# Optimization experiments

Measured on AMD Instinct MI355X. Metric: run time of the kernel, lower is better.

The kernel has to match this reference:

```python
import jax, jax.numpy as jnp
import numpy as np


def setup_inputs() -> dict:
    key = jax.random.key(0)
    k1, k2, k3, k4 = jax.random.split(key, 4)
    N, Ck, Cv, T, H, W = 8, 128, 512, 8, 30, 30
    return {
        "q_key": jax.random.normal(k1, (N, Ck, H, W), dtype=jnp.float32),
        "q_val": jax.random.normal(k2, (N, Cv, H, W), dtype=jnp.float32),
        "m_key": jax.random.normal(k3, (N, Ck, T, H, W), dtype=jnp.float32),
        "m_val": jax.random.normal(k4, (N, Cv, T, H, W), dtype=jnp.float32),
    }


def reference(q_key, q_val, m_key, m_val):
    N, Ck, H, W = q_key.shape
    _, Cv, T, Hm, Wm = m_val.shape
    qk = q_key.reshape(N, Ck, H * W)            # n c q
    mk = m_key.reshape(N, Ck, T * Hm * Wm)      # n c m
    # affinity [n, q, m], scaled by 1/sqrt(Ck)
    aff = jnp.einsum("ncq,ncm->nqm", qk, mk) * (Ck ** -0.5)
    # NOTE: softmax over the QUERY axis (axis=1), per the original module
    attn = jax.nn.softmax(aff, axis=1)
    mv = m_val.reshape(N, Cv, T * Hm * Wm)      # n c m
    mapped = jnp.einsum("nqm,ncm->ncq", attn, mv).reshape(N, Cv, Hm, Wm)
    return jnp.concatenate([q_val, mapped], axis=1)  # [N, 2*Cv, H, W]
```

## Files before the change

kernel.cpp:

```cpp
#include <hip/hip_runtime.h>
#include <stdint.h>

#define N_  8
#define CK  128
#define CV  512
#define HW  900
#define M_  7200
#define QK_SCALE 0.08838834764831845f

typedef __attribute__((ext_vector_type(8))) short  short8;
typedef __attribute__((ext_vector_type(4))) float  floatx4;
typedef __attribute__((ext_vector_type(4))) unsigned int   uintx4;
typedef __attribute__((ext_vector_type(4))) unsigned short ushortx4;

__device__ __forceinline__ uint16_t f32_to_bf16(float x) {
    union { float f; uint32_t u; } v; v.f = x;
    return (uint16_t)((v.u + 0x7FFFu + ((v.u >> 16) & 1u)) >> 16);
}

__device__ __forceinline__ void gload_lds16(const uint16_t* g, short* l) {
    __builtin_amdgcn_global_load_lds(
        (const __attribute__((address_space(1))) void*)g,
        (__attribute__((address_space(3))) void*)l,
        16, 0, 0);
}

#define WAITV(n) asm volatile("s_waitcnt vmcnt(" #n ")" ::: "memory")
#define BARRIER() do { __builtin_amdgcn_sched_barrier(0); \
                       __builtin_amdgcn_s_barrier(); \
                       __builtin_amdgcn_sched_barrier(0); } while (0)

__global__ void k_zero(float* __restrict__ p) {
    int i = blockIdx.x * 256 + threadIdx.x;
    if (i < N_ * M_) p[i] = 0.f;
}

__global__ __launch_bounds__(256) void k_copy_qval(const float* __restrict__ qv,
                                                   float* __restrict__ out) {
    unsigned i = blockIdx.x * 256 + threadIdx.x;
    unsigned e = i * 4u;
    unsigned n = e / (CV * HW);
    unsigned off = e - n * (CV * HW);
    *(floatx4*)&out[(size_t)n * (2 * CV * HW) + off] = *(const floatx4*)&qv[e];
}

__global__ __launch_bounds__(256) void k_trans(const float* __restrict__ in,
                                               uint16_t* __restrict__ outp, int L) {
    __shared__ float tile[32][33];
    const int tx = threadIdx.x & 31;
    const int ty = threadIdx.x >> 5;
    const int l0 = blockIdx.x * 32;
    const int c0 = blockIdx.y * 32;
    const int n  = blockIdx.z;
    const float* src = in + (size_t)n * CK * L;
    uint16_t* dst = outp + (size_t)n * L * CK;
#pragma unroll
    for (int p = 0; p < 4; p++) {
        int c = c0 + p * 8 + ty;
        int l = l0 + tx;
        float v = 0.f;
        if (l < L) v = src[(size_t)c * L + l];
        tile[p * 8 + ty][tx] = v;
    }
    __syncthreads();
#pragma unroll
    for (int p = 0; p < 4; p++) {
        int l = l0 + p * 8 + ty;
        int c = c0 + tx;
        if (l < L) dst[(size_t)l * CK + c] = f32_to_bf16(tile[tx][p * 8 + ty]);
    }
}

#define K1_TS 144

__global__ __launch_bounds__(256) void k1_gemm_exp(
    const uint16_t* __restrict__ qkT,
    const uint16_t* __restrict__ mkT,
    uint16_t* __restrict__ E,
    float* __restrict__ dsum)
{
    __shared__ __align__(16) short smem[32768];
    __shared__ float colsum[128];

    const int bid = blockIdx.x + 57 * (blockIdx.y + 8 * blockIdx.z);
    const int swz = (bid & 7) * 456 + (bid >> 3);
    const int mb   = swz % 57;
    const int rest = swz / 57;
    const int m0 = mb * 128;
    const int q0 = (rest & 7) * 128;
    const int n  = rest >> 3;
    const int tid = threadIdx.x;

    if (tid < 128) colsum[tid] = 0.f;

    const int lane = tid & 63;
    const int wid  = tid >> 6;
    const int wq   = (wid >> 1) << 6;
    const int wm   = (wid & 1) << 6;
    const int fr   = lane & 15;
    const int quad = lane >> 4;

    const int ca = wid * 2;
    const int rr = lane >> 2;
    const int cc = (lane & 3) * 8;

    const uint16_t* Ab = qkT + (size_t)n * HW * CK;
    const uint16_t* Bb = mkT + (size_t)n * M_ * CK;
    const uint16_t* A0p = Ab + (size_t)(q0 + ca * 16 + rr) * CK + cc;
    const uint16_t* A1p = A0p + 16 * CK;
    const uint16_t* B0p = Bb + (size_t)(m0 + ca * 16 + rr) * CK + cc;
    const uint16_t* B1p = B0p + 16 * CK;

    floatx4 acc[4][4];
#pragma unroll
    for (int a = 0; a < 4; a++)
#pragma unroll
        for (int b = 0; b < 4; b++) acc[a][b] = (floatx4){0.f, 0.f, 0.f, 0.f};

#define K1_STAGE(buf, ko) do { \
    short* dA = smem + (buf) * 8192 + ca * 512; \
    short* dB = dA + 4096; \
    gload_lds16(A0p + (ko), dA); \
    gload_lds16(A1p + (ko), dA + 512); \
    gload_lds16(B0p + (ko), dB); \
    gload_lds16(B1p + (ko), dB + 512); \
} while (0)

#define K1_COMPUTE(buf) do { \
    const short* bA = smem + (buf) * 8192; \
    const short* bB = bA + 4096; \
    const int k0 = quad * 8; \
    short8 af[4], bfr[4]; \
    _Pragma("unroll") \
    for (int t = 0; t < 4; t++) \
        af[t] = *(const short8*)&bA[(wq + t * 16 + fr) * 32 + k0]; \
    _Pragma("unroll") \
    for (int t = 0; t < 4; t++) \
        bfr[t] = *(const short8*)&bB[(wm + t * 16 + fr) * 32 + k0]; \
    _Pragma("unroll") \
    for (int tq = 0; tq < 4; tq++) \
        _Pragma("unroll") \
        for (int tm = 0; tm < 4; tm++) \
            acc[tq][tm] = __builtin_amdgcn_mfma_f32_16x16x32_bf16( \
                af[tq], bfr[tm], acc[tq][tm], 0, 0, 0); \
} while (0)

    K1_STAGE(0, 0); K1_STAGE(1, 32); K1_STAGE(2, 64);
    WAITV(8); BARRIER(); K1_STAGE(3, 96); K1_COMPUTE(0);
    WAITV(8); BARRIER(); K1_COMPUTE(1);
    WAITV(4); BARRIER(); K1_COMPUTE(2);
    WAITV(0); BARRIER(); K1_COMPUTE(3);

    __syncthreads();
    float cs[4] = {0.f, 0.f, 0.f, 0.f};
#pragma unroll
    for (int tq = 0; tq < 4; tq++) {
#pragma unroll
        for (int tm = 0; tm < 4; tm++) {
            const int col = wm + tm * 16 + fr;
#pragma unroll
            for (int i = 0; i < 4; i++) {
                const int row = wq + tq * 16 + quad * 4 + i;
                float e = __expf(acc[tq][tm][i] * QK_SCALE);
                if (q0 + row < HW) cs[tm] += e;
                smem[row * K1_TS + col] = (short)f32_to_bf16(e);
            }
        }
    }
#pragma unroll
    for (int tm = 0; tm < 4; tm++) {
        float s = cs[tm];
        s += __shfl_xor(s, 16, 64);
        s += __shfl_xor(s, 32, 64);
        if (quad == 0) atomicAdd(&colsum[wm + tm * 16 + fr], s);
    }
    __syncthreads();

    uint16_t* En = E + (size_t)n * HW * M_;
#pragma unroll
    for (int j = 0; j < 8; j++) {
        int idx = tid + j * 256;
        int r   = idx >> 4;
        int c8  = (idx & 15) * 8;
        if (q0 + r < HW && m0 + c8 + 8 <= M_) {
            uintx4 v = *(const uintx4*)&smem[r * K1_TS + c8];
            *(uintx4*)&En[(size_t)(q0 + r) * M_ + m0 + c8] = v;
        }
    }
    if (tid < 128) {
        const int gm = m0 + tid;
        if (gm < M_) atomicAdd(&dsum[(size_t)n * M_ + gm], colsum[tid]);
    }
#undef K1_STAGE
#undef K1_COMPUTE
}

__global__ __launch_bounds__(256) void k_mvs(
    const float* __restrict__ mval,
    const float* __restrict__ dsum,
    uint16_t* __restrict__ mvs)
{
    unsigned i = blockIdx.x * 256 + threadIdx.x;
    unsigned base = i * 4u;
    unsigned n = base / (unsigned)(CV * M_);
    unsigned m = base % (unsigned)M_;
    floatx4 v = *(const floatx4*)&mval[base];
    floatx4 d = *(const floatx4*)&dsum[n * (unsigned)M_ + m];
    ushortx4 o;
    o[0] = f32_to_bf16(v[0] * (1.0f / d[0]));
    o[1] = f32_to_bf16(v[1] * (1.0f / d[1]));
    o[2] = f32_to_bf16(v[2] * (1.0f / d[2]));
    o[3] = f32_to_bf16(v[3] * (1.0f / d[3]));
    *(ushortx4*)&mvs[base] = o;
}

#define K2_NT 225

__global__ __launch_bounds__(256) void k2_hyb(
    const uint16_t* __restrict__ mvs,
    const uint16_t* __restrict__ E,
    float* __restrict__ out)
{
    __shared__ __align__(16) short ldsA[3 * 4096];

    const int bid = blockIdx.x + 8 * (blockIdx.y + 4 * blockIdx.z);
    const int swz = (bid & 7) * 32 + (bid >> 3);
    const int c0 = (swz & 3) << 7;
    const int q0 = ((swz >> 2) & 7) << 7;
    const int n  = swz >> 5;

    const int tid  = threadIdx.x;
    const int lane = tid & 63;
    const int wid  = tid >> 6;
    const int wc   = (wid >> 1) << 6;
    const int wq   = (wid & 1) << 6;
    const int fr   = lane & 15;
    const int quad = lane >> 4;

    const int ca = wid * 2;
    const int rr = lane >> 2;
    const int cc = (lane & 3) * 8;
    const uint16_t* A0p = mvs + (size_t)(n * CV + c0 + ca * 16 + rr) * M_ + cc;
    const uint16_t* A1p = A0p + (size_t)16 * M_;

    const uint16_t* En = E + (size_t)n * HW * M_;
    const uint16_t* Bp0 = En + (size_t)(q0 + wq +  0 + fr) * M_ + quad * 8;
    const uint16_t* Bp1 = En + (size_t)(q0 + wq + 16 + fr) * M_ + quad * 8;
    const uint16_t* Bp2 = En + (size_t)(q0 + wq + 32 + fr) * M_ + quad * 8;
    const uint16_t* Bp3 = En + (size_t)(q0 + wq + 48 + fr) * M_ + quad * 8;

    floatx4 acc[4][4];
#pragma unroll
    for (int a = 0; a < 4; a++)
#pragma unroll
        for (int b = 0; b < 4; b++) acc[a][b] = (floatx4){0.f, 0.f, 0.f, 0.f};

    short8 breg0[4], breg1[4], breg2[4];

#define K2_STAGE_A(buf, mo) do { \
    gload_lds16(A0p + (mo), ldsA + (buf) * 4096 + ca * 512); \
    gload_lds16(A1p + (mo), ldsA + (buf) * 4096 + ca * 512 + 512); \
} while (0)

#define K2_LOAD_B(brg, mo) do { \
    brg[0] = *(const short8*)(Bp0 + (mo)); \
    brg[1] = *(const short8*)(Bp1 + (mo)); \
    brg[2] = *(const short8*)(Bp2 + (mo)); \
    brg[3] = *(const short8*)(Bp3 + (mo)); \
} while (0)

#define K2_COMPUTE(bA, brg) do { \
    const short* pA = ldsA + (bA) * 4096; \
    short8 af[4]; \
    _Pragma("unroll") \
    for (int t = 0; t < 4; t++) \
        af[t] = *(const short8*)&pA[(wc + t * 16 + fr) * 32 + quad * 8]; \
    _Pragma("unroll") \
    for (int tc = 0; tc < 4; tc++) \
        _Pragma("unroll") \
        for (int tq = 0; tq < 4; tq++) \
            acc[tc][tq] = __builtin_amdgcn_mfma_f32_16x16x32_bf16( \
                af[tc], brg[tq], acc[tc][tq], 0, 0, 0); \
} while (0)

    K2_STAGE_A(0, 0);  K2_LOAD_B(breg0, 0);
    K2_STAGE_A(1, 32); K2_LOAD_B(breg1, 32);

    int mo = 64;
    for (int s = 0; s < 74; s++) {
        WAITV(10); BARRIER();
        K2_STAGE_A(2, mo); K2_LOAD_B(breg2, mo); K2_COMPUTE(0, breg0);
        mo += 32;
        WAITV(10); BARRIER();
        K2_STAGE_A(0, mo); K2_LOAD_B(breg0, mo); K2_COMPUTE(1, breg1);
        mo += 32;
        WAITV(10); BARRIER();
        K2_STAGE_A(1, mo); K2_LOAD_B(breg1, mo); K2_COMPUTE(2, breg2);
        mo += 32;
    }
    WAITV(10); BARRIER();
    K2_STAGE_A(2, mo); K2_LOAD_B(breg2, mo); K2_COMPUTE(0, breg0);
    WAITV(10); BARRIER();
    K2_COMPUTE(1, breg1);
    WAITV(4); BARRIER();
    K2_COMPUTE(2, breg2);

    float* On = out + (size_t)n * (2 * CV * HW) + (size_t)CV * HW;
#pragma unroll
    for (int tc = 0; tc < 4; tc++) {
#pragma unroll
        for (int tq = 0; tq < 4; tq++) {
            const int gq = q0 + wq + tq * 16 + fr;
            if (gq < HW) {
#pragma unroll
                for (int i = 0; i < 4; i++) {
                    const int gc = c0 + wc + tc * 16 + quad * 4 + i;
                    On[(size_t)gc * HW + gq] = acc[tc][tq][i];
                }
            }
        }
    }
#undef K2_STAGE_A
#undef K2_LOAD_B
#undef K2_COMPUTE
}

extern "C" void kernel_launch(void* const* d_in, const int* in_sizes, int n_in,
                              void* d_out, int out_size, void* d_ws, size_t ws_size,
                              hipStream_t stream) {
    const float* qkey = (const float*)d_in[0];
    const float* qval = (const float*)d_in[1];
    const float* mkey = (const float*)d_in[2];
    const float* mval = (const float*)d_in[3];
    float* out = (float*)d_out;

    char* ws = (char*)d_ws;
    uint16_t* E        = (uint16_t*)ws;
    float*    dsum     = (float*)(ws + 103680000);
    uint16_t* mvs      = (uint16_t*)(ws + 104140800);
    uint16_t* qkT      = (uint16_t*)(ws + 163123200);
    uint16_t* mkT      = (uint16_t*)(ws + 163123200 + 1843200);

    (void)in_sizes; (void)n_in; (void)out_size; (void)ws_size;

    k_zero<<<dim3((N_ * M_ + 255) / 256), 256, 0, stream>>>(dsum);
    k_copy_qval<<<dim3((N_ * CV * HW) / 4 / 256), 256, 0, stream>>>(qval, out);
    k_trans<<<dim3(29, 4, N_), 256, 0, stream>>>(qkey, qkT, HW);
    k_trans<<<dim3(225, 4, N_), 256, 0, stream>>>(mkey, mkT, M_);
    k1_gemm_exp<<<dim3(57, 8, N_), 256, 0, stream>>>(qkT, mkT, E, dsum);
    k_mvs<<<dim3((N_ * CV * M_) / 4 / 256), 256, 0, stream>>>(mval, dsum, mvs);
    k2_hyb<<<dim3(8, 4, 8), 256, 0, stream>>>(mvs, E, out);
}
```

Baseline: 471.9 us.

## Split second GEMM along M into three partials and fuse prep kernels

The second GEMM (attention times values) launched only 256 blocks, so it is now split along the memory dimension into three chunks of 2400. Each chunk writes fp32 partials to workspace, and a new reduce kernel sums them into the output. That gives 768 blocks for better occupancy across the many CUs, at the cost of extra partial write/read traffic and one more launch. Separately, the zero, copy and two transpose kernels are merged into one launch to cut launch overhead. The partials buffer reuses the qkT/mkT workspace region, which is safe because those are consumed before k2 runs.

Result: faster. 431.5 us (-8.6%).

```diff
diff --git a/kernel.cpp b/kernel.cpp
--- a/kernel.cpp
+++ b/kernel.cpp
@@ -30,30 +30,16 @@
                        __builtin_amdgcn_s_barrier(); \
                        __builtin_amdgcn_sched_barrier(0); } while (0)
 
-__global__ void k_zero(float* __restrict__ p) {
-    int i = blockIdx.x * 256 + threadIdx.x;
-    if (i < N_ * M_) p[i] = 0.f;
-}
-
-__global__ __launch_bounds__(256) void k_copy_qval(const float* __restrict__ qv,
-                                                   float* __restrict__ out) {
-    unsigned i = blockIdx.x * 256 + threadIdx.x;
-    unsigned e = i * 4u;
-    unsigned n = e / (CV * HW);
-    unsigned off = e - n * (CV * HW);
-    *(floatx4*)&out[(size_t)n * (2 * CV * HW) + off] = *(const floatx4*)&qv[e];
-}
-
-__global__ __launch_bounds__(256) void k_trans(const float* __restrict__ in,
-                                               uint16_t* __restrict__ outp, int L) {
+__device__ __forceinline__ void trans_body(const float* __restrict__ in,
+                                           uint16_t* __restrict__ outp, int L,
+                                           int bx, int by, int bz, int tid) {
     __shared__ float tile[32][33];
-    const int tx = threadIdx.x & 31;
-    const int ty = threadIdx.x >> 5;
-    const int l0 = blockIdx.x * 32;
-    const int c0 = blockIdx.y * 32;
-    const int n  = blockIdx.z;
-    const float* src = in + (size_t)n * CK * L;
-    uint16_t* dst = outp + (size_t)n * L * CK;
+    const int tx = tid & 31;
+    const int ty = tid >> 5;
+    const int l0 = bx * 32;
+    const int c0 = by * 32;
+    const float* src = in + (size_t)bz * CK * L;
+    uint16_t* dst = outp + (size_t)bz * L * CK;
 #pragma unroll
     for (int p = 0; p < 4; p++) {
         int c = c0 + p * 8 + ty;
@@ -68,6 +54,33 @@
         int l = l0 + p * 8 + ty;
         int c = c0 + tx;
         if (l < L) dst[(size_t)l * CK + c] = f32_to_bf16(tile[tx][p * 8 + ty]);
+    }
+}
+
+__global__ __launch_bounds__(256) void k_prep(
+    const float* __restrict__ qkey, const float* __restrict__ mkey,
+    const float* __restrict__ qval, float* __restrict__ out,
+    uint16_t* __restrict__ qkT, uint16_t* __restrict__ mkT,
+    float* __restrict__ dsum)
+{
+    const int b = blockIdx.x;
+    const int tid = threadIdx.x;
+    if (b < 928) {
+        trans_body(qkey, qkT, HW, b % 29, (b / 29) & 3, b / 116, tid);
+    } else if (b < 8128) {
+        const int bb = b - 928;
+        trans_body(mkey, mkT, M_, bb % 225, (bb / 225) & 3, bb / 900, tid);
+    } else if (b < 11728) {
+        const int bb = b - 8128;
+        unsigned i = (unsigned)bb * 256 + tid;
+        unsigned e = i * 4u;
+        unsigned n = e / (CV * HW);
+        unsigned off = e - n * (CV * HW);
+        *(floatx4*)&out[(size_t)n * (2 * CV * HW) + off] = *(const floatx4*)&qval[e];
+    } else {
+        const int bb = b - 11728;
+        int i = bb * 256 + tid;
+        if (i < N_ * M_) dsum[i] = 0.f;
     }
 }
 
@@ -214,20 +227,24 @@
     *(ushortx4*)&mvs[base] = o;
 }
 
-#define K2_NT 225
-
-__global__ __launch_bounds__(256) void k2_hyb(
+#define K2_SPLITS 3
+#define K2_BK 32
+#define K2_STEPS 75
+
+__global__ __launch_bounds__(256, 3) void k2_split3b(
     const uint16_t* __restrict__ mvs,
     const uint16_t* __restrict__ E,
-    float* __restrict__ out)
+    float* __restrict__ partials)
 {
     __shared__ __align__(16) short ldsA[3 * 4096];
 
     const int bid = blockIdx.x + 8 * (blockIdx.y + 4 * blockIdx.z);
-    const int swz = (bid & 7) * 32 + (bid >> 3);
+    const int swz = (bid & 7) * 96 + (bid >> 3);
     const int c0 = (swz & 3) << 7;
     const int q0 = ((swz >> 2) & 7) << 7;
-    const int n  = swz >> 5;
+    const int nz = swz >> 5;
+    const int n     = nz / K2_SPLITS;
+    const int split = nz - n * K2_SPLITS;
 
     const int tid  = threadIdx.x;
     const int lane = tid & 63;
@@ -240,10 +257,11 @@
     const int ca = wid * 2;
     const int rr = lane >> 2;
     const int cc = (lane & 3) * 8;
-    const uint16_t* A0p = mvs + (size_t)(n * CV + c0 + ca * 16 + rr) * M_ + cc;
+    const uint16_t* A0p = mvs + (size_t)(n * CV + c0 + ca * 16 + rr) * M_
+                              + split * 2400 + cc;
     const uint16_t* A1p = A0p + (size_t)16 * M_;
 
-    const uint16_t* En = E + (size_t)n * HW * M_;
+    const uint16_t* En = E + (size_t)n * HW * M_ + split * 2400;
     const uint16_t* Bp0 = En + (size_t)(q0 + wq +  0 + fr) * M_ + quad * 8;
     const uint16_t* Bp1 = En + (size_t)(q0 + wq + 16 + fr) * M_ + quad * 8;
     const uint16_t* Bp2 = En + (size_t)(q0 + wq + 32 + fr) * M_ + quad * 8;
@@ -287,7 +305,7 @@
     K2_STAGE_A(1, 32); K2_LOAD_B(breg1, 32);
 
     int mo = 64;
-    for (int s = 0; s < 74; s++) {
+    for (int s = 0; s < 24; s++) {
         WAITV(10); BARRIER();
         K2_STAGE_A(2, mo); K2_LOAD_B(breg2, mo); K2_COMPUTE(0, breg0);
         mo += 32;
@@ -305,7 +323,7 @@
     WAITV(4); BARRIER();
     K2_COMPUTE(2, breg2);
 
-    float* On = out + (size_t)n * (2 * CV * HW) + (size_t)CV * HW;
+    float* P = partials + ((size_t)split * N_ + n) * CV * HW;
 #pragma unroll
     for (int tc = 0; tc < 4; tc++) {
 #pragma unroll
@@ -315,7 +333,7 @@
 #pragma unroll
                 for (int i = 0; i < 4; i++) {
                     const int gc = c0 + wc + tc * 16 + quad * 4 + i;
-                    On[(size_t)gc * HW + gq] = acc[tc][tq][i];
+                    P[(size_t)gc * HW + gq] = acc[tc][tq][i];
                 }
             }
         }
@@ -323,6 +341,21 @@
 #undef K2_STAGE_A
 #undef K2_LOAD_B
 #undef K2_COMPUTE
+}
+
+__global__ __launch_bounds__(256) void k_reduce3(const float* __restrict__ partials,
+                                                 float* __restrict__ out) {
+    unsigned i = blockIdx.x * 256 + threadIdx.x;
+    unsigned e = i * 4u;
+    unsigned n = e / (CV * HW);
+    unsigned off = e - n * (CV * HW);
+    const size_t stride = (size_t)N_ * CV * HW;
+    const float* p = partials + (size_t)n * CV * HW + off;
+    floatx4 a = *(const floatx4*)&p[0];
+    floatx4 b = *(const floatx4*)&p[stride];
+    floatx4 c = *(const floatx4*)&p[2 * stride];
+    floatx4 s = a + b + c;
+    *(floatx4*)&out[(size_t)n * (2 * CV * HW) + CV * HW + off] = s;
 }
 
 extern "C" void kernel_launch(void* const* d_in, const int* in_sizes, int n_in,
@@ -338,16 +371,15 @@
     uint16_t* E        = (uint16_t*)ws;
     float*    dsum     = (float*)(ws + 103680000);
     uint16_t* mvs      = (uint16_t*)(ws + 104140800);
+    float*    partials = (float*)(ws + 163123200);
     uint16_t* qkT      = (uint16_t*)(ws + 163123200);
     uint16_t* mkT      = (uint16_t*)(ws + 163123200 + 1843200);
 
     (void)in_sizes; (void)n_in; (void)out_size; (void)ws_size;
 
-    k_zero<<<dim3((N_ * M_ + 255) / 256), 256, 0, stream>>>(dsum);
-    k_copy_qval<<<dim3((N_ * CV * HW) / 4 / 256), 256, 0, stream>>>(qval, out);
-    k_trans<<<dim3(29, 4, N_), 256, 0, stream>>>(qkey, qkT, HW);
-    k_trans<<<dim3(225, 4, N_), 256, 0, stream>>>(mkey, mkT, M_);
+    k_prep<<<dim3(11953), 256, 0, stream>>>(qkey, mkey, qval, out, qkT, mkT, dsum);
     k1_gemm_exp<<<dim3(57, 8, N_), 256, 0, stream>>>(qkT, mkT, E, dsum);
     k_mvs<<<dim3((N_ * CV * M_) / 4 / 256), 256, 0, stream>>>(mval, dsum, mvs);
-    k2_hyb<<<dim3(8, 4, 8), 256, 0, stream>>>(mvs, E, out);
-}
+    k2_split3b<<<dim3(8, 4, N_ * K2_SPLITS), 256, 0, stream>>>(mvs, E, partials);
+    k_reduce3<<<dim3((N_ * CV * HW) / 4 / 256), 256, 0, stream>>>(partials, out);
+}
```
